# Kernel optimization log

Hardware: AMD Instinct MI355X
Metric: run time of the kernel (lower is better)

Reference implementation:

```python
import jax, jax.numpy as jnp
import numpy as np

B, T, D_IN, HID, D_OUT = 16, 4096, 256, 512, 256


def setup_inputs() -> dict:
    key = jax.random.key(0)
    k0, k1, k2, k3 = jax.random.split(key, 4)
    x = jax.random.normal(k0, (B, T, D_IN), dtype=jnp.float32)
    # nn.Linear default init ~ U(-1/sqrt(fan_in), 1/sqrt(fan_in)); approximate with scaled normal
    W_in = jax.random.normal(k1, (HID, D_IN), dtype=jnp.float32) / np.sqrt(D_IN)
    # hidden_ff.weight is explicitly set to diag(rand(hid_dim)) in the module
    W_h = jnp.diag(jax.random.uniform(k2, (HID,), dtype=jnp.float32))
    W_out = jax.random.normal(k3, (D_OUT, HID), dtype=jnp.float32) / np.sqrt(HID)
    return {"x": x, "W_in": W_in, "W_h": W_h, "W_out": W_out}


def reference(x, W_in, W_h, W_out):
    # x: [B, T, D_in]; W_in: [H, D_in]; W_h: [H, H]; W_out: [D_out, H]
    xp = jnp.einsum('btd,hd->bth', x, W_in)  # input projection, [B, T, H]

    def step(h, xt):
        # h_t = x_t + h_{t-1} @ W_h^T  (linear recurrence, h_0 = 0)
        h_next = xt + h @ W_h.T
        return h_next, h_next

    h0 = jnp.zeros((x.shape[0], W_h.shape[0]), dtype=x.dtype)
    _, hs = jax.lax.scan(step, h0, jnp.swapaxes(xp, 0, 1))  # hs: [T, B, H]
    hs = jnp.swapaxes(hs, 0, 1)  # [B, T, H]
    return jnp.einsum('bth,oh->bto', hs, W_out)  # [B, T, D_out]
```

## Files before the change

kernel.cpp:

```cpp
#include <hip/hip_runtime.h>
#include <hip/hip_bf16.h>
#include <stdint.h>

#define BATCH 16
#define SEQT  4096
#define DIN   256
#define HID   512
#define DOUT  256
#define M_TOT 65536
#define CLEN  128
#define NCHUNK 32

typedef short bf16x8 __attribute__((ext_vector_type(8)));
typedef float f32x4  __attribute__((ext_vector_type(4)));
typedef unsigned short u16;
typedef unsigned short u16x4 __attribute__((ext_vector_type(4)));
typedef unsigned int uint32;

__device__ __forceinline__ void ld_lds16(const void* g, void* l) {
    __builtin_amdgcn_global_load_lds(
        (const __attribute__((address_space(1))) void*)g,
        (__attribute__((address_space(3))) void*)l, 16, 0, 0);
}

__device__ __forceinline__ u16 f2bf_rne(float f) {
    uint32 v = __float_as_uint(f);
    v += 0x7FFFu + ((v >> 16) & 1u);
    return (u16)(v >> 16);
}

__device__ __forceinline__ float bf2f(u16 s) {
    return __uint_as_float((uint32)s << 16);
}

__device__ __forceinline__ void splitf(float f, u16& hi, u16& lo) {
    const uint32 u = __float_as_uint(f);
    hi = (u16)(u >> 16);
    lo = f2bf_rne(f - __uint_as_float(u & 0xFFFF0000u));
}

__global__ __launch_bounds__(256) void prep(
        const float* __restrict__ Wh, const float* __restrict__ Win,
        const float* __restrict__ Wout, float* __restrict__ wdiag,
        float* __restrict__ wpow, u16* __restrict__ Winhi,
        u16* __restrict__ Winlo, u16* __restrict__ Wouthi,
        u16* __restrict__ Woutlo) {
    const int bid = blockIdx.x, tid = threadIdx.x;
    if (bid == 0) {
        for (int h = tid; h < HID; h += 256) {
            const float wv = Wh[(size_t)h * HID + h];
            wdiag[h] = wv;
            float p = 1.f;
            for (int t = 0; t < CLEN; ++t) { p *= wv; wpow[t * HID + h] = p; }
        }
    } else if (bid <= 128) {
        const int f4 = (bid - 1) * 256 + tid;
        const f32x4 v = *(const f32x4*)(Win + (size_t)f4 * 4);
        u16x4 hv, lv;
#pragma unroll
        for (int k = 0; k < 4; ++k) { u16 a, b; splitf(v[k], a, b); hv[k] = a; lv[k] = b; }
        *(u16x4*)(Winhi + (size_t)f4 * 4) = hv;
        *(u16x4*)(Winlo + (size_t)f4 * 4) = lv;
    } else {
        const int f4 = (bid - 129) * 256 + tid;
        const f32x4 v = *(const f32x4*)(Wout + (size_t)f4 * 4);
        u16x4 hv, lv;
#pragma unroll
        for (int k = 0; k < 4; ++k) { u16 a, b; splitf(v[k], a, b); hv[k] = a; lv[k] = b; }
        *(u16x4*)(Wouthi + (size_t)f4 * 4) = hv;
        *(u16x4*)(Woutlo + (size_t)f4 * 4) = lv;
    }
}

__global__ __launch_bounds__(256, 2) void gemm1_scan(
        const float* __restrict__ X, const u16* __restrict__ Whi,
        const u16* __restrict__ Wlo, u16* __restrict__ localbf,
        float* __restrict__ L, const float* __restrict__ wdiag,
        const float* __restrict__ wpow) {
    __shared__ __align__(16) char smem[75776];
    u16*   Ah = (u16*)smem;
    u16*   Al = (u16*)(smem + 16384);
    u16*   Bh = (u16*)(smem + 32768);
    u16*   Bl = (u16*)(smem + 49152);
    float* st = (float*)smem;
    float* segT = (float*)(smem + 67584);
    float* segC = (float*)(smem + 71680);

    const int tid  = threadIdx.x;
    const int w    = tid >> 6;
    const int lane = tid & 63;

    const int bid  = blockIdx.x;
    const int xcd  = bid & 7;
    const int slot = bid >> 3;
    const int mBase = (xcd * 64 + (slot >> 2)) * 128;
    const int nBase = (slot & 3) * 128;

    const int wr = w >> 1, wc = w & 1;
    const int fr = lane & 15;
    const int kg = lane >> 4;

    const int bRow = lane >> 3;
    const int bCol = ((lane & 7) ^ bRow) * 8;

    f32x4 acc[4][4];
#pragma unroll
    for (int i = 0; i < 4; ++i)
#pragma unroll
        for (int j = 0; j < 4; ++j) acc[i][j] = (f32x4){0.f, 0.f, 0.f, 0.f};

    for (int k0 = 0; k0 < DIN; k0 += 64) {
#pragma unroll
        for (int i = 0; i < 4; ++i) {
            const int c = w * 4 + i;
            const int r = c * 8 + bRow;
            ld_lds16(Whi + (size_t)(nBase + r) * DIN + k0 + bCol, Bh + c * 512);
            ld_lds16(Wlo + (size_t)(nBase + r) * DIN + k0 + bCol, Bl + c * 512);
        }
#pragma unroll
        for (int it = 0; it < 4; ++it) {
            const int idx = it * 256 + tid;
            const int r  = idx >> 3;
            const int gl = idx & 7;
            const float* src = X + (size_t)(mBase + r) * DIN + k0 + gl * 8;
            const f32x4 v0 = *(const f32x4*)(src);
            const f32x4 v1 = *(const f32x4*)(src + 4);
            bf16x8 h8, l8;
#pragma unroll
            for (int e = 0; e < 4; ++e) {
                u16 a, b;
                splitf(v0[e], a, b); h8[e] = (short)a; l8[e] = (short)b;
                splitf(v1[e], a, b); h8[e + 4] = (short)a; l8[e + 4] = (short)b;
            }
            const int phys = r * 64 + ((gl ^ (r & 7)) * 8);
            *(bf16x8*)(Ah + phys) = h8;
            *(bf16x8*)(Al + phys) = l8;
        }
        __syncthreads();
#pragma unroll
        for (int ks = 0; ks < 2; ++ks) {
            const int colE = ks * 32 + kg * 8;
            bf16x8 ah[4], al[4], bh[4], bl[4];
#pragma unroll
            for (int f = 0; f < 4; ++f) {
                const int ra = wr * 64 + f * 16 + fr;
                const int pa = ra * 64 + (colE ^ ((fr & 7) << 3));
                ah[f] = *(const bf16x8*)(Ah + pa);
                al[f] = *(const bf16x8*)(Al + pa);
                const int rb = wc * 64 + f * 16 + fr;
                const int pb = rb * 64 + (colE ^ ((fr & 7) << 3));
                bh[f] = *(const bf16x8*)(Bh + pb);
                bl[f] = *(const bf16x8*)(Bl + pb);
            }
#pragma unroll
            for (int i = 0; i < 4; ++i)
#pragma unroll
                for (int j = 0; j < 4; ++j) {
                    acc[i][j] = __builtin_amdgcn_mfma_f32_16x16x32_bf16(ah[i], bh[j], acc[i][j], 0, 0, 0);
                    acc[i][j] = __builtin_amdgcn_mfma_f32_16x16x32_bf16(ah[i], bl[j], acc[i][j], 0, 0, 0);
                    acc[i][j] = __builtin_amdgcn_mfma_f32_16x16x32_bf16(al[i], bh[j], acc[i][j], 0, 0, 0);
                }
        }
        __syncthreads();
    }

#pragma unroll
    for (int i = 0; i < 4; ++i)
#pragma unroll
        for (int j = 0; j < 4; ++j)
#pragma unroll
            for (int rg = 0; rg < 4; ++rg)
                st[(wr * 64 + i * 16 + kg * 4 + rg) * 132 + wc * 64 + j * 16 + fr]
                    = acc[i][j][rg];
    __syncthreads();

    const int sseg = tid >> 5;
    const int cg   = (tid & 31) * 4;
    const f32x4 wv4 = *(const f32x4*)(wdiag + nBase + cg);

    f32x4 rr[16];
    {
        f32x4 run = (f32x4){0.f, 0.f, 0.f, 0.f};
#pragma unroll
        for (int i = 0; i < 16; ++i) {
            const f32x4 v = *(const f32x4*)&st[(sseg * 16 + i) * 132 + cg];
#pragma unroll
            for (int e = 0; e < 4; ++e) run[e] = fmaf(wv4[e], run[e], v[e]);
            rr[i] = run;
        }
        *(f32x4*)&segT[sseg * 128 + cg] = run;
    }
    __syncthreads();

    if (tid < 32) {
        const int c4 = tid * 4;
        const f32x4 w16 = *(const f32x4*)(wpow + 15 * HID + nBase + c4);
        f32x4 c = (f32x4){0.f, 0.f, 0.f, 0.f};
#pragma unroll
        for (int s2 = 0; s2 < 8; ++s2) {
            *(f32x4*)&segC[s2 * 128 + c4] = c;
            const f32x4 tv = *(const f32x4*)&segT[s2 * 128 + c4];
#pragma unroll
            for (int e = 0; e < 4; ++e) c[e] = fmaf(w16[e], c[e], tv[e]);
        }
        const int cI = (mBase >> 7) & (NCHUNK - 1);
        const int bI = mBase >> 12;
        *(f32x4*)&L[(cI * BATCH + bI) * HID + nBase + c4] = c;
    }
    __syncthreads();

    {
        const f32x4 cin = *(const f32x4*)&segC[sseg * 128 + cg];
        f32x4 p = wv4;
        u16* dst = localbf + (size_t)(mBase + sseg * 16) * HID + nBase + cg;
#pragma unroll
        for (int i = 0; i < 16; ++i) {
            u16x4 ob;
#pragma unroll
            for (int e = 0; e < 4; ++e)
                ob[e] = f2bf_rne(fmaf(p[e], cin[e], rr[i][e]));
            *(u16x4*)(dst + (size_t)i * HID) = ob;
#pragma unroll
            for (int e = 0; e < 4; ++e) p[e] *= wv4[e];
        }
    }
}

__global__ __launch_bounds__(256) void scan_carry(
        const float* __restrict__ L, const float* __restrict__ wpow,
        float* __restrict__ carry) {
    const int idx = blockIdx.x * 256 + threadIdx.x;
    const int h = idx & (HID - 1);
    const int b = idx >> 9;
    const float wf = wpow[(CLEN - 1) * HID + h];
    float H = 0.f;
    for (int c = 0; c < NCHUNK; ++c) {
        const int o = (c * BATCH + b) * HID + h;
        carry[o] = H;
        H = fmaf(wf, H, L[o]);
    }
}

__global__ __launch_bounds__(256, 2) void gemm2_fix(
        const u16* __restrict__ localbf, const u16* __restrict__ Bhi_g,
        const u16* __restrict__ Blo_g, const float* __restrict__ wpow,
        const float* __restrict__ carry, float* __restrict__ C) {
    __shared__ __align__(16) char smem[65536];
    u16* Ah = (u16*)smem;
    u16* Al = (u16*)(smem + 16384);
    u16* Bh = (u16*)(smem + 32768);
    u16* Bl = (u16*)(smem + 49152);

    const int tid  = threadIdx.x;
    const int w    = tid >> 6;
    const int lane = tid & 63;

    const int bid  = blockIdx.x;
    const int xcd  = bid & 7;
    const int slot = bid >> 3;
    const int mBase = (xcd * 64 + (slot >> 1)) * 128;
    const int nBase = (slot & 1) * 128;

    const int wr = w >> 1, wc = w & 1;
    const int fr = lane & 15;
    const int kg = lane >> 4;

    const int bRow = lane >> 3;
    const int bCol = ((lane & 7) ^ bRow) * 8;

    const int cI = (mBase >> 7) & (NCHUNK - 1);
    const int bI = mBase >> 12;
    const float* crow = carry + (size_t)(cI * BATCH + bI) * HID;

    f32x4 acc[4][4];
#pragma unroll
    for (int i = 0; i < 4; ++i)
#pragma unroll
        for (int j = 0; j < 4; ++j) acc[i][j] = (f32x4){0.f, 0.f, 0.f, 0.f};

    for (int k0 = 0; k0 < HID; k0 += 64) {
#pragma unroll
        for (int i = 0; i < 4; ++i) {
            const int c = w * 4 + i;
            const int r2 = c * 8 + bRow;
            ld_lds16(Bhi_g + (size_t)(nBase + r2) * HID + k0 + bCol, Bh + c * 512);
            ld_lds16(Blo_g + (size_t)(nBase + r2) * HID + k0 + bCol, Bl + c * 512);
        }
#pragma unroll
        for (int it = 0; it < 4; ++it) {
            const int idx = it * 256 + tid;
            const int r  = idx >> 3;
            const int gl = idx & 7;
            const int gm = mBase + r;
            const size_t col = (size_t)(k0 + gl * 8);
            const bf16x8 lv = *(const bf16x8*)(localbf + (size_t)gm * HID + col);
            const f32x4 p0 = *(const f32x4*)(wpow + (size_t)r * HID + col);
            const f32x4 p1 = *(const f32x4*)(wpow + (size_t)r * HID + col + 4);
            const f32x4 c0 = *(const f32x4*)(crow + col);
            const f32x4 c1 = *(const f32x4*)(crow + col + 4);
            bf16x8 h8, l8;
#pragma unroll
            for (int e = 0; e < 4; ++e) {
                const float f0 = fmaf(p0[e], c0[e], bf2f((u16)lv[e]));
                const float f1 = fmaf(p1[e], c1[e], bf2f((u16)lv[e + 4]));
                u16 a, b;
                splitf(f0, a, b); h8[e] = (short)a; l8[e] = (short)b;
                splitf(f1, a, b); h8[e + 4] = (short)a; l8[e + 4] = (short)b;
            }
            const int phys = r * 64 + ((gl ^ (r & 7)) * 8);
            *(bf16x8*)(Ah + phys) = h8;
            *(bf16x8*)(Al + phys) = l8;
        }
        __syncthreads();
#pragma unroll
        for (int ks = 0; ks < 2; ++ks) {
            const int colE = ks * 32 + kg * 8;
            bf16x8 ah[4], al[4], bh[4], bl[4];
#pragma unroll
            for (int f = 0; f < 4; ++f) {
                const int ra = wr * 64 + f * 16 + fr;
                const int pa = ra * 64 + (colE ^ ((fr & 7) << 3));
                ah[f] = *(const bf16x8*)(Ah + pa);
                al[f] = *(const bf16x8*)(Al + pa);
                const int rb = wc * 64 + f * 16 + fr;
                const int pb = rb * 64 + (colE ^ ((fr & 7) << 3));
                bh[f] = *(const bf16x8*)(Bh + pb);
                bl[f] = *(const bf16x8*)(Bl + pb);
            }
#pragma unroll
            for (int i = 0; i < 4; ++i)
#pragma unroll
                for (int j = 0; j < 4; ++j) {
                    acc[i][j] = __builtin_amdgcn_mfma_f32_16x16x32_bf16(ah[i], bh[j], acc[i][j], 0, 0, 0);
                    acc[i][j] = __builtin_amdgcn_mfma_f32_16x16x32_bf16(ah[i], bl[j], acc[i][j], 0, 0, 0);
                    acc[i][j] = __builtin_amdgcn_mfma_f32_16x16x32_bf16(al[i], bh[j], acc[i][j], 0, 0, 0);
                }
        }
        __syncthreads();
    }

#pragma unroll
    for (int i = 0; i < 4; ++i) {
        const size_t row0 = (size_t)mBase + wr * 64 + i * 16 + kg * 4;
#pragma unroll
        for (int j = 0; j < 4; ++j) {
            const int col = nBase + wc * 64 + j * 16 + fr;
#pragma unroll
            for (int rg = 0; rg < 4; ++rg)
                C[(row0 + rg) * DOUT + col] = acc[i][j][rg];
        }
    }
}

extern "C" void kernel_launch(void* const* d_in, const int* in_sizes, int n_in,
                              void* d_out, int out_size, void* d_ws, size_t ws_size,
                              hipStream_t stream) {
    const float* x     = (const float*)d_in[0];
    const float* W_in  = (const float*)d_in[1];
    const float* W_h   = (const float*)d_in[2];
    const float* W_out = (const float*)d_in[3];
    float* out = (float*)d_out;

    char* ws = (char*)d_ws;
    u16*   localbf = (u16*)(ws);
    float* L       = (float*)(ws + 134217728);
    float* carry   = (float*)(ws + 135266304);
    float* wpow    = (float*)(ws + 136314880);
    float* wdiag   = (float*)(ws + 136577024);
    u16*   Winhi   = (u16*)(ws + 136579072);
    u16*   Winlo   = (u16*)(ws + 136841216);
    u16*   Wouthi  = (u16*)(ws + 137103360);
    u16*   Woutlo  = (u16*)(ws + 137365504);

    prep<<<257, 256, 0, stream>>>(W_h, W_in, W_out, wdiag, wpow,
                                  Winhi, Winlo, Wouthi, Woutlo);
    gemm1_scan<<<2048, 256, 0, stream>>>(x, Winhi, Winlo, localbf, L, wdiag, wpow);
    scan_carry<<<32, 256, 0, stream>>>(L, wpow, carry);
    gemm2_fix<<<1024, 256, 0, stream>>>(localbf, Wouthi, Woutlo, wpow, carry, out);
}
```

Before: 128.0 us.

## Register-prefetch next K tile in gemm1 and compute segment carries redundantly per thread

Replaces the direct global-to-LDS loads of the weight tiles and the synchronous X load/split with a register prefetch. The next K slice is loaded into registers while MFMA runs on the current slice, which is meant to overlap global latency with compute. It also removes the single-warp carry pass and its extra barrier: every thread recomputes the 8-segment carry chain from segT and picks its own incoming carry, which drops the segC buffer and shrinks LDS. The cost is higher register pressure from the prefetch buffers under launch_bounds(256,2), plus some redundant carry arithmetic.

```diff
diff --git a/kernel.cpp b/kernel.cpp
--- a/kernel.cpp
+++ b/kernel.cpp
@@ -77,14 +77,13 @@
         const u16* __restrict__ Wlo, u16* __restrict__ localbf,
         float* __restrict__ L, const float* __restrict__ wdiag,
         const float* __restrict__ wpow) {
-    __shared__ __align__(16) char smem[75776];
+    __shared__ __align__(16) char smem[71680];
     u16*   Ah = (u16*)smem;
     u16*   Al = (u16*)(smem + 16384);
     u16*   Bh = (u16*)(smem + 32768);
     u16*   Bl = (u16*)(smem + 49152);
     float* st = (float*)smem;
     float* segT = (float*)(smem + 67584);
-    float* segC = (float*)(smem + 71680);
 
     const int tid  = threadIdx.x;
     const int w    = tid >> 6;
@@ -109,34 +108,56 @@
 #pragma unroll
         for (int j = 0; j < 4; ++j) acc[i][j] = (f32x4){0.f, 0.f, 0.f, 0.f};
 
-    for (int k0 = 0; k0 < DIN; k0 += 64) {
+    f32x4 ap0[4], ap1[4];
+    bf16x8 bhp[4], blp[4];
+
+    auto LOADK = [&](int k0) {
 #pragma unroll
         for (int i = 0; i < 4; ++i) {
             const int c = w * 4 + i;
             const int r = c * 8 + bRow;
-            ld_lds16(Whi + (size_t)(nBase + r) * DIN + k0 + bCol, Bh + c * 512);
-            ld_lds16(Wlo + (size_t)(nBase + r) * DIN + k0 + bCol, Bl + c * 512);
+            bhp[i] = *(const bf16x8*)(Whi + (size_t)(nBase + r) * DIN + k0 + bCol);
+            blp[i] = *(const bf16x8*)(Wlo + (size_t)(nBase + r) * DIN + k0 + bCol);
         }
 #pragma unroll
         for (int it = 0; it < 4; ++it) {
             const int idx = it * 256 + tid;
-            const int r  = idx >> 3;
-            const int gl = idx & 7;
+            const int r = idx >> 3, gl = idx & 7;
             const float* src = X + (size_t)(mBase + r) * DIN + k0 + gl * 8;
-            const f32x4 v0 = *(const f32x4*)(src);
-            const f32x4 v1 = *(const f32x4*)(src + 4);
+            ap0[it] = *(const f32x4*)(src);
+            ap1[it] = *(const f32x4*)(src + 4);
+        }
+    };
+    auto WRITEK = [&]() {
+#pragma unroll
+        for (int i = 0; i < 4; ++i) {
+            const int c = w * 4 + i;
+            *(bf16x8*)(Bh + c * 512 + lane * 8) = bhp[i];
+            *(bf16x8*)(Bl + c * 512 + lane * 8) = blp[i];
+        }
+#pragma unroll
+        for (int it = 0; it < 4; ++it) {
+            const int idx = it * 256 + tid;
+            const int r = idx >> 3, gl = idx & 7;
             bf16x8 h8, l8;
 #pragma unroll
             for (int e = 0; e < 4; ++e) {
                 u16 a, b;
-                splitf(v0[e], a, b); h8[e] = (short)a; l8[e] = (short)b;
-                splitf(v1[e], a, b); h8[e + 4] = (short)a; l8[e + 4] = (short)b;
+                splitf(ap0[it][e], a, b); h8[e] = (short)a; l8[e] = (short)b;
+                splitf(ap1[it][e], a, b); h8[e + 4] = (short)a; l8[e + 4] = (short)b;
             }
             const int phys = r * 64 + ((gl ^ (r & 7)) * 8);
             *(bf16x8*)(Ah + phys) = h8;
             *(bf16x8*)(Al + phys) = l8;
         }
+    };
+
+    LOADK(0);
+#pragma unroll
+    for (int kk = 0; kk < 4; ++kk) {
+        WRITEK();
         __syncthreads();
+        if (kk < 3) LOADK((kk + 1) * 64);
 #pragma unroll
         for (int ks = 0; ks < 2; ++ks) {
             const int colE = ks * 32 + kg * 8;
@@ -192,25 +213,22 @@
     }
     __syncthreads();
 
-    if (tid < 32) {
-        const int c4 = tid * 4;
-        const f32x4 w16 = *(const f32x4*)(wpow + 15 * HID + nBase + c4);
+    {
+        const f32x4 w16 = *(const f32x4*)(wpow + 15 * HID + nBase + cg);
         f32x4 c = (f32x4){0.f, 0.f, 0.f, 0.f};
-#pragma unroll
-        for (int s2 = 0; s2 < 8; ++s2) {
-            *(f32x4*)&segC[s2 * 128 + c4] = c;
-            const f32x4 tv = *(const f32x4*)&segT[s2 * 128 + c4];
+        f32x4 cin = (f32x4){0.f, 0.f, 0.f, 0.f};
+#pragma unroll
+        for (int s = 0; s < 8; ++s) {
+            if (s == sseg) cin = c;
+            const f32x4 tv = *(const f32x4*)&segT[s * 128 + cg];
 #pragma unroll
             for (int e = 0; e < 4; ++e) c[e] = fmaf(w16[e], c[e], tv[e]);
         }
-        const int cI = (mBase >> 7) & (NCHUNK - 1);
-        const int bI = mBase >> 12;
-        *(f32x4*)&L[(cI * BATCH + bI) * HID + nBase + c4] = c;
-    }
-    __syncthreads();
-
-    {
-        const f32x4 cin = *(const f32x4*)&segC[sseg * 128 + cg];
+        if (sseg == 7) {
+            const int cI = (mBase >> 7) & (NCHUNK - 1);
+            const int bI = mBase >> 12;
+            *(f32x4*)&L[(cI * BATCH + bI) * HID + nBase + cg] = c;
+        }
         f32x4 p = wv4;
         u16* dst = localbf + (size_t)(mBase + sseg * 16) * HID + nBase + cg;
 #pragma unroll
```

Measured after the change: 129.5 us. Within noise of the previous version (+1.2%).

## Do chunk scan in registers with shuffles, shrink LDS for higher occupancy

Applied to the files above, without the earlier changes.

The K-step drops from 64 to 32, which halves the A/B LDS tiles, and the fp32 staging tile is replaced by a bf16 one. Total shared memory falls from about 74KB to about 35KB and the launch bound rises to 4 blocks per CU. The intra-chunk diagonal recurrence now runs directly on MFMA accumulator registers, using lane shuffles and precomputed powers of w, with a single cross-warp carry passed through LDS. The bf16 output is written through a staging buffer so global stores are coalesced. In exchange there are more loop iterations and barriers, extra register pressure from the power arrays, and numerical differences in how the powers are computed.

```diff
diff --git a/kernel.cpp b/kernel.cpp
--- a/kernel.cpp
+++ b/kernel.cpp
@@ -38,6 +38,8 @@
     hi = (u16)(u >> 16);
     lo = f2bf_rne(f - __uint_as_float(u & 0xFFFF0000u));
 }
+
+__device__ __forceinline__ int sfun(int r) { return (r ^ (r >> 2)) & 3; }
 
 __global__ __launch_bounds__(256) void prep(
         const float* __restrict__ Wh, const float* __restrict__ Win,
@@ -72,19 +74,17 @@
     }
 }
 
-__global__ __launch_bounds__(256, 2) void gemm1_scan(
+__global__ __launch_bounds__(256, 4) void gemm1_scan(
         const float* __restrict__ X, const u16* __restrict__ Whi,
         const u16* __restrict__ Wlo, u16* __restrict__ localbf,
-        float* __restrict__ L, const float* __restrict__ wdiag,
-        const float* __restrict__ wpow) {
-    __shared__ __align__(16) char smem[75776];
-    u16*   Ah = (u16*)smem;
-    u16*   Al = (u16*)(smem + 16384);
-    u16*   Bh = (u16*)(smem + 32768);
-    u16*   Bl = (u16*)(smem + 49152);
-    float* st = (float*)smem;
-    float* segT = (float*)(smem + 67584);
-    float* segC = (float*)(smem + 71680);
+        float* __restrict__ L, const float* __restrict__ wdiag) {
+    __shared__ __align__(16) char smem[35328];
+    u16*   Ah  = (u16*)smem;
+    u16*   Al  = (u16*)(smem + 8192);
+    u16*   Bh  = (u16*)(smem + 16384);
+    u16*   Bl  = (u16*)(smem + 24576);
+    u16*   stb = (u16*)smem;
+    float* xw  = (float*)(smem + 34816);
 
     const int tid  = threadIdx.x;
     const int w    = tid >> 6;
@@ -100,8 +100,13 @@
     const int fr = lane & 15;
     const int kg = lane >> 4;
 
-    const int bRow = lane >> 3;
-    const int bCol = ((lane & 7) ^ bRow) * 8;
+    const int r_a = tid >> 1;
+    const int h_a = tid & 1;
+    const int s_a = sfun(r_a);
+
+    const int rl  = lane >> 2;
+    const int pg  = lane & 3;
+    const int lgb = pg ^ sfun(rl);
 
     f32x4 acc[4][4];
 #pragma unroll
@@ -109,119 +114,147 @@
 #pragma unroll
         for (int j = 0; j < 4; ++j) acc[i][j] = (f32x4){0.f, 0.f, 0.f, 0.f};
 
-    for (int k0 = 0; k0 < DIN; k0 += 64) {
-#pragma unroll
-        for (int i = 0; i < 4; ++i) {
-            const int c = w * 4 + i;
-            const int r = c * 8 + bRow;
-            ld_lds16(Whi + (size_t)(nBase + r) * DIN + k0 + bCol, Bh + c * 512);
-            ld_lds16(Wlo + (size_t)(nBase + r) * DIN + k0 + bCol, Bl + c * 512);
-        }
-#pragma unroll
-        for (int it = 0; it < 4; ++it) {
-            const int idx = it * 256 + tid;
-            const int r  = idx >> 3;
-            const int gl = idx & 7;
-            const float* src = X + (size_t)(mBase + r) * DIN + k0 + gl * 8;
+    for (int kk = 0; kk < 8; ++kk) {
+        const int k0 = kk * 32;
+#pragma unroll
+        for (int i = 0; i < 2; ++i) {
+            const int c = w * 2 + i;
+            const int row = nBase + c * 16 + rl;
+            ld_lds16(Whi + (size_t)row * DIN + k0 + lgb * 8, Bh + c * 512);
+            ld_lds16(Wlo + (size_t)row * DIN + k0 + lgb * 8, Bl + c * 512);
+        }
+        {
+            const float* src = X + (size_t)(mBase + r_a) * DIN + k0 + h_a * 16;
             const f32x4 v0 = *(const f32x4*)(src);
             const f32x4 v1 = *(const f32x4*)(src + 4);
-            bf16x8 h8, l8;
+            const f32x4 v2 = *(const f32x4*)(src + 8);
+            const f32x4 v3 = *(const f32x4*)(src + 12);
+            bf16x8 h0, l0, h1, l1;
 #pragma unroll
             for (int e = 0; e < 4; ++e) {
                 u16 a, b;
-                splitf(v0[e], a, b); h8[e] = (short)a; l8[e] = (short)b;
-                splitf(v1[e], a, b); h8[e + 4] = (short)a; l8[e + 4] = (short)b;
-            }
-            const int phys = r * 64 + ((gl ^ (r & 7)) * 8);
-            *(bf16x8*)(Ah + phys) = h8;
-            *(bf16x8*)(Al + phys) = l8;
+                splitf(v0[e], a, b); h0[e] = (short)a; l0[e] = (short)b;
+                splitf(v1[e], a, b); h0[e + 4] = (short)a; l0[e + 4] = (short)b;
+                splitf(v2[e], a, b); h1[e] = (short)a; l1[e] = (short)b;
+                splitf(v3[e], a, b); h1[e + 4] = (short)a; l1[e + 4] = (short)b;
+            }
+            u16* arow = Ah + r_a * 32;
+            u16* arol = Al + r_a * 32;
+            const int g0 = (2 * h_a) ^ s_a, g1 = (2 * h_a + 1) ^ s_a;
+            *(bf16x8*)(arow + g0 * 8) = h0;
+            *(bf16x8*)(arow + g1 * 8) = h1;
+            *(bf16x8*)(arol + g0 * 8) = l0;
+            *(bf16x8*)(arol + g1 * 8) = l1;
         }
         __syncthreads();
-#pragma unroll
-        for (int ks = 0; ks < 2; ++ks) {
-            const int colE = ks * 32 + kg * 8;
-            bf16x8 ah[4], al[4], bh[4], bl[4];
-#pragma unroll
-            for (int f = 0; f < 4; ++f) {
-                const int ra = wr * 64 + f * 16 + fr;
-                const int pa = ra * 64 + (colE ^ ((fr & 7) << 3));
-                ah[f] = *(const bf16x8*)(Ah + pa);
-                al[f] = *(const bf16x8*)(Al + pa);
-                const int rb = wc * 64 + f * 16 + fr;
-                const int pb = rb * 64 + (colE ^ ((fr & 7) << 3));
-                bh[f] = *(const bf16x8*)(Bh + pb);
-                bl[f] = *(const bf16x8*)(Bl + pb);
-            }
-#pragma unroll
-            for (int i = 0; i < 4; ++i)
-#pragma unroll
-                for (int j = 0; j < 4; ++j) {
-                    acc[i][j] = __builtin_amdgcn_mfma_f32_16x16x32_bf16(ah[i], bh[j], acc[i][j], 0, 0, 0);
-                    acc[i][j] = __builtin_amdgcn_mfma_f32_16x16x32_bf16(ah[i], bl[j], acc[i][j], 0, 0, 0);
-                    acc[i][j] = __builtin_amdgcn_mfma_f32_16x16x32_bf16(al[i], bh[j], acc[i][j], 0, 0, 0);
-                }
-        }
+
+        const int sfr = sfun(fr);
+        bf16x8 ah[4], al[4], bh[4], bl[4];
+#pragma unroll
+        for (int f = 0; f < 4; ++f) {
+            const int sa = (wr * 64 + f * 16 + fr) * 32 + ((kg ^ sfr) * 8);
+            ah[f] = *(const bf16x8*)(Ah + sa);
+            al[f] = *(const bf16x8*)(Al + sa);
+            const int sb = (wc * 64 + f * 16 + fr) * 32 + ((kg ^ sfr) * 8);
+            bh[f] = *(const bf16x8*)(Bh + sb);
+            bl[f] = *(const bf16x8*)(Bl + sb);
+        }
+#pragma unroll
+        for (int i = 0; i < 4; ++i)
+#pragma unroll
+            for (int j = 0; j < 4; ++j) {
+                acc[i][j] = __builtin_amdgcn_mfma_f32_16x16x32_bf16(ah[i], bh[j], acc[i][j], 0, 0, 0);
+                acc[i][j] = __builtin_amdgcn_mfma_f32_16x16x32_bf16(ah[i], bl[j], acc[i][j], 0, 0, 0);
+                acc[i][j] = __builtin_amdgcn_mfma_f32_16x16x32_bf16(al[i], bh[j], acc[i][j], 0, 0, 0);
+            }
         __syncthreads();
     }
 
-#pragma unroll
-    for (int i = 0; i < 4; ++i)
-#pragma unroll
-        for (int j = 0; j < 4; ++j)
-#pragma unroll
-            for (int rg = 0; rg < 4; ++rg)
-                st[(wr * 64 + i * 16 + kg * 4 + rg) * 132 + wc * 64 + j * 16 + fr]
-                    = acc[i][j][rg];
+    float w1[4], w2[4], w3[4], w4[4], w8[4], w16[4];
+#pragma unroll
+    for (int j = 0; j < 4; ++j) {
+        const float wv = wdiag[nBase + wc * 64 + j * 16 + fr];
+        w1[j] = wv; w2[j] = wv * wv; w3[j] = w2[j] * wv; w4[j] = w2[j] * w2[j];
+        w8[j] = w4[j] * w4[j]; w16[j] = w8[j] * w8[j];
+    }
+    float Bst[4] = {0.f, 0.f, 0.f, 0.f};
+#pragma unroll
+    for (int i = 0; i < 4; ++i) {
+#pragma unroll
+        for (int j = 0; j < 4; ++j) {
+            const float l0 = acc[i][j][0];
+            const float l1 = fmaf(w1[j], l0, acc[i][j][1]);
+            const float l2 = fmaf(w1[j], l1, acc[i][j][2]);
+            const float l3 = fmaf(w1[j], l2, acc[i][j][3]);
+            const float x0 = __shfl(l3, fr);
+            const float x1 = __shfl(l3, fr + 16);
+            const float x2 = __shfl(l3, fr + 32);
+            const float x3 = __shfl(l3, fr + 48);
+            float s = Bst[j];
+            float S = s;
+            s = fmaf(w4[j], s, x0); S = (kg == 1) ? s : S;
+            s = fmaf(w4[j], s, x1); S = (kg == 2) ? s : S;
+            s = fmaf(w4[j], s, x2); S = (kg == 3) ? s : S;
+            s = fmaf(w4[j], s, x3);
+            Bst[j] = s;
+            acc[i][j][0] = fmaf(w1[j], S, l0);
+            acc[i][j][1] = fmaf(w2[j], S, l1);
+            acc[i][j][2] = fmaf(w3[j], S, l2);
+            acc[i][j][3] = fmaf(w4[j], S, l3);
+        }
+    }
+    if (wr == 0 && kg == 0) {
+#pragma unroll
+        for (int j = 0; j < 4; ++j) xw[wc * 64 + j * 16 + fr] = Bst[j];
+    }
     __syncthreads();
-
-    const int sseg = tid >> 5;
-    const int cg   = (tid & 31) * 4;
-    const f32x4 wv4 = *(const f32x4*)(wdiag + nBase + cg);
-
-    f32x4 rr[16];
-    {
-        f32x4 run = (f32x4){0.f, 0.f, 0.f, 0.f};
-#pragma unroll
-        for (int i = 0; i < 16; ++i) {
-            const f32x4 v = *(const f32x4*)&st[(sseg * 16 + i) * 132 + cg];
-#pragma unroll
-            for (int e = 0; e < 4; ++e) run[e] = fmaf(wv4[e], run[e], v[e]);
-            rr[i] = run;
-        }
-        *(f32x4*)&segT[sseg * 128 + cg] = run;
-    }
-    __syncthreads();
-
-    if (tid < 32) {
-        const int c4 = tid * 4;
-        const f32x4 w16 = *(const f32x4*)(wpow + 15 * HID + nBase + c4);
-        f32x4 c = (f32x4){0.f, 0.f, 0.f, 0.f};
-#pragma unroll
-        for (int s2 = 0; s2 < 8; ++s2) {
-            *(f32x4*)&segC[s2 * 128 + c4] = c;
-            const f32x4 tv = *(const f32x4*)&segT[s2 * 128 + c4];
-#pragma unroll
-            for (int e = 0; e < 4; ++e) c[e] = fmaf(w16[e], c[e], tv[e]);
-        }
+    if (wr == 1) {
         const int cI = (mBase >> 7) & (NCHUNK - 1);
         const int bI = mBase >> 12;
-        *(f32x4*)&L[(cI * BATCH + bI) * HID + nBase + c4] = c;
+#pragma unroll
+        for (int j = 0; j < 4; ++j) {
+            const float cin = xw[wc * 64 + j * 16 + fr];
+            float wkg = 1.f;
+            if (kg & 1) wkg *= w4[j];
+            if (kg & 2) wkg *= w8[j];
+            float f = wkg;
+#pragma unroll
+            for (int i = 0; i < 4; ++i) {
+                const float g = f * cin;
+                acc[i][j][0] = fmaf(w1[j], g, acc[i][j][0]);
+                acc[i][j][1] = fmaf(w2[j], g, acc[i][j][1]);
+                acc[i][j][2] = fmaf(w3[j], g, acc[i][j][2]);
+                acc[i][j][3] = fmaf(w4[j], g, acc[i][j][3]);
+                f *= w16[j];
+            }
+            if (kg == 0) {
+                const float w32 = w16[j] * w16[j];
+                const float w64 = w32 * w32;
+                L[(cI * BATCH + bI) * HID + nBase + wc * 64 + j * 16 + fr]
+                    = fmaf(w64, cin, Bst[j]);
+            }
+        }
     }
     __syncthreads();
 
+#pragma unroll
+    for (int i = 0; i < 4; ++i)
+#pragma unroll
+        for (int j = 0; j < 4; ++j)
+#pragma unroll
+            for (int rg = 0; rg < 4; ++rg)
+                stb[(wr * 64 + i * 16 + kg * 4 + rg) * 136
+                    + wc * 64 + j * 16 + fr] = f2bf_rne(acc[i][j][rg]);
+    __syncthreads();
+
     {
-        const f32x4 cin = *(const f32x4*)&segC[sseg * 128 + cg];
-        f32x4 p = wv4;
-        u16* dst = localbf + (size_t)(mBase + sseg * 16) * HID + nBase + cg;
-#pragma unroll
-        for (int i = 0; i < 16; ++i) {
-            u16x4 ob;
-#pragma unroll
-            for (int e = 0; e < 4; ++e)
-                ob[e] = f2bf_rne(fmaf(p[e], cin[e], rr[i][e]));
-            *(u16x4*)(dst + (size_t)i * HID) = ob;
-#pragma unroll
-            for (int e = 0; e < 4; ++e) p[e] *= wv4[e];
+        const int rr2 = tid >> 4;
+        const int cl  = (tid & 15) * 8;
+#pragma unroll
+        for (int p = 0; p < 8; ++p) {
+            const int row = p * 16 + rr2;
+            const bf16x8 v = *(const bf16x8*)(stb + row * 136 + cl);
+            *(bf16x8*)(localbf + (size_t)(mBase + row) * HID + nBase + cl) = v;
         }
     }
 }
@@ -374,7 +407,7 @@
 
     prep<<<257, 256, 0, stream>>>(W_h, W_in, W_out, wdiag, wpow,
                                   Winhi, Winlo, Wouthi, Woutlo);
-    gemm1_scan<<<2048, 256, 0, stream>>>(x, Winhi, Winlo, localbf, L, wdiag, wpow);
+    gemm1_scan<<<2048, 256, 0, stream>>>(x, Winhi, Winlo, localbf, L, wdiag);
     scan_carry<<<32, 256, 0, stream>>>(L, wpow, carry);
     gemm2_fix<<<1024, 256, 0, stream>>>(localbf, Wouthi, Woutlo, wpow, carry, out);
 }
```

Measured after the change: 156.6 us. +22.4%, slower.

## Double gemm1_scan block to 512 threads with 16-step scan segments

Applied to the files above, without the earlier changes.

Raises gemm1_scan from 256 to 512 threads per block. Each wave now covers a 64x32 output tile instead of 64x64, and the chunk scan is split into 16 segments of 8 rows instead of 8 segments of 16. The serial carry pass that only 32 threads ran is replaced by every thread redundantly scanning the 16 segment totals, which removes one barrier and the segC buffer. The aim is more waves per CU and a shorter serial scan, at the cost of less register reuse per wave in the MFMA loop and redundant carry arithmetic.

```diff
diff --git a/kernel.cpp b/kernel.cpp
--- a/kernel.cpp
+++ b/kernel.cpp
@@ -72,7 +72,7 @@
     }
 }
 
-__global__ __launch_bounds__(256, 2) void gemm1_scan(
+__global__ __launch_bounds__(512, 2) void gemm1_scan(
         const float* __restrict__ X, const u16* __restrict__ Whi,
         const u16* __restrict__ Wlo, u16* __restrict__ localbf,
         float* __restrict__ L, const float* __restrict__ wdiag,
@@ -84,7 +84,6 @@
     u16*   Bl = (u16*)(smem + 49152);
     float* st = (float*)smem;
     float* segT = (float*)(smem + 67584);
-    float* segC = (float*)(smem + 71680);
 
     const int tid  = threadIdx.x;
     const int w    = tid >> 6;
@@ -96,30 +95,31 @@
     const int mBase = (xcd * 64 + (slot >> 2)) * 128;
     const int nBase = (slot & 3) * 128;
 
-    const int wr = w >> 1, wc = w & 1;
+    const int wr = w >> 2;
+    const int wc = w & 3;
     const int fr = lane & 15;
     const int kg = lane >> 4;
 
     const int bRow = lane >> 3;
     const int bCol = ((lane & 7) ^ bRow) * 8;
 
-    f32x4 acc[4][4];
+    f32x4 acc[4][2];
 #pragma unroll
     for (int i = 0; i < 4; ++i)
 #pragma unroll
-        for (int j = 0; j < 4; ++j) acc[i][j] = (f32x4){0.f, 0.f, 0.f, 0.f};
+        for (int j = 0; j < 2; ++j) acc[i][j] = (f32x4){0.f, 0.f, 0.f, 0.f};
 
     for (int k0 = 0; k0 < DIN; k0 += 64) {
 #pragma unroll
-        for (int i = 0; i < 4; ++i) {
-            const int c = w * 4 + i;
+        for (int i = 0; i < 2; ++i) {
+            const int c = w * 2 + i;
             const int r = c * 8 + bRow;
             ld_lds16(Whi + (size_t)(nBase + r) * DIN + k0 + bCol, Bh + c * 512);
             ld_lds16(Wlo + (size_t)(nBase + r) * DIN + k0 + bCol, Bl + c * 512);
         }
 #pragma unroll
-        for (int it = 0; it < 4; ++it) {
-            const int idx = it * 256 + tid;
+        for (int it = 0; it < 2; ++it) {
+            const int idx = it * 512 + tid;
             const int r  = idx >> 3;
             const int gl = idx & 7;
             const float* src = X + (size_t)(mBase + r) * DIN + k0 + gl * 8;
@@ -140,22 +140,25 @@
 #pragma unroll
         for (int ks = 0; ks < 2; ++ks) {
             const int colE = ks * 32 + kg * 8;
-            bf16x8 ah[4], al[4], bh[4], bl[4];
+            bf16x8 ah[4], al[4], bh[2], bl[2];
 #pragma unroll
             for (int f = 0; f < 4; ++f) {
                 const int ra = wr * 64 + f * 16 + fr;
                 const int pa = ra * 64 + (colE ^ ((fr & 7) << 3));
                 ah[f] = *(const bf16x8*)(Ah + pa);
                 al[f] = *(const bf16x8*)(Al + pa);
-                const int rb = wc * 64 + f * 16 + fr;
+            }
+#pragma unroll
+            for (int j = 0; j < 2; ++j) {
+                const int rb = wc * 32 + j * 16 + fr;
                 const int pb = rb * 64 + (colE ^ ((fr & 7) << 3));
-                bh[f] = *(const bf16x8*)(Bh + pb);
-                bl[f] = *(const bf16x8*)(Bl + pb);
+                bh[j] = *(const bf16x8*)(Bh + pb);
+                bl[j] = *(const bf16x8*)(Bl + pb);
             }
 #pragma unroll
             for (int i = 0; i < 4; ++i)
 #pragma unroll
-                for (int j = 0; j < 4; ++j) {
+                for (int j = 0; j < 2; ++j) {
                     acc[i][j] = __builtin_amdgcn_mfma_f32_16x16x32_bf16(ah[i], bh[j], acc[i][j], 0, 0, 0);
                     acc[i][j] = __builtin_amdgcn_mfma_f32_16x16x32_bf16(ah[i], bl[j], acc[i][j], 0, 0, 0);
                     acc[i][j] = __builtin_amdgcn_mfma_f32_16x16x32_bf16(al[i], bh[j], acc[i][j], 0, 0, 0);
@@ -167,10 +170,10 @@
 #pragma unroll
     for (int i = 0; i < 4; ++i)
 #pragma unroll
-        for (int j = 0; j < 4; ++j)
+        for (int j = 0; j < 2; ++j)
 #pragma unroll
             for (int rg = 0; rg < 4; ++rg)
-                st[(wr * 64 + i * 16 + kg * 4 + rg) * 132 + wc * 64 + j * 16 + fr]
+                st[(wr * 64 + i * 16 + kg * 4 + rg) * 132 + wc * 32 + j * 16 + fr]
                     = acc[i][j][rg];
     __syncthreads();
 
@@ -178,12 +181,12 @@
     const int cg   = (tid & 31) * 4;
     const f32x4 wv4 = *(const f32x4*)(wdiag + nBase + cg);
 
-    f32x4 rr[16];
+    f32x4 rr[8];
     {
         f32x4 run = (f32x4){0.f, 0.f, 0.f, 0.f};
 #pragma unroll
-        for (int i = 0; i < 16; ++i) {
-            const f32x4 v = *(const f32x4*)&st[(sseg * 16 + i) * 132 + cg];
+        for (int i = 0; i < 8; ++i) {
+            const f32x4 v = *(const f32x4*)&st[(sseg * 8 + i) * 132 + cg];
 #pragma unroll
             for (int e = 0; e < 4; ++e) run[e] = fmaf(wv4[e], run[e], v[e]);
             rr[i] = run;
@@ -192,29 +195,26 @@
     }
     __syncthreads();
 
-    if (tid < 32) {
-        const int c4 = tid * 4;
-        const f32x4 w16 = *(const f32x4*)(wpow + 15 * HID + nBase + c4);
+    {
+        const f32x4 w8 = *(const f32x4*)(wpow + 7 * HID + nBase + cg);
         f32x4 c = (f32x4){0.f, 0.f, 0.f, 0.f};
-#pragma unroll
-        for (int s2 = 0; s2 < 8; ++s2) {
-            *(f32x4*)&segC[s2 * 128 + c4] = c;
-            const f32x4 tv = *(const f32x4*)&segT[s2 * 128 + c4];
-#pragma unroll
-            for (int e = 0; e < 4; ++e) c[e] = fmaf(w16[e], c[e], tv[e]);
-        }
-        const int cI = (mBase >> 7) & (NCHUNK - 1);
-        const int bI = mBase >> 12;
-        *(f32x4*)&L[(cI * BATCH + bI) * HID + nBase + c4] = c;
-    }
-    __syncthreads();
-
-    {
-        const f32x4 cin = *(const f32x4*)&segC[sseg * 128 + cg];
+        f32x4 cin = (f32x4){0.f, 0.f, 0.f, 0.f};
+#pragma unroll
+        for (int s = 0; s < 16; ++s) {
+            if (s == sseg) cin = c;
+            const f32x4 tv = *(const f32x4*)&segT[s * 128 + cg];
+#pragma unroll
+            for (int e = 0; e < 4; ++e) c[e] = fmaf(w8[e], c[e], tv[e]);
+        }
+        if (sseg == 15) {
+            const int cI = (mBase >> 7) & (NCHUNK - 1);
+            const int bI = mBase >> 12;
+            *(f32x4*)&L[(cI * BATCH + bI) * HID + nBase + cg] = c;
+        }
         f32x4 p = wv4;
-        u16* dst = localbf + (size_t)(mBase + sseg * 16) * HID + nBase + cg;
-#pragma unroll
-        for (int i = 0; i < 16; ++i) {
+        u16* dst = localbf + (size_t)(mBase + sseg * 8) * HID + nBase + cg;
+#pragma unroll
+        for (int i = 0; i < 8; ++i) {
             u16x4 ob;
 #pragma unroll
             for (int e = 0; e < 4; ++e)
@@ -374,7 +374,7 @@
 
     prep<<<257, 256, 0, stream>>>(W_h, W_in, W_out, wdiag, wpow,
                                   Winhi, Winlo, Wouthi, Woutlo);
-    gemm1_scan<<<2048, 256, 0, stream>>>(x, Winhi, Winlo, localbf, L, wdiag, wpow);
+    gemm1_scan<<<2048, 512, 0, stream>>>(x, Winhi, Winlo, localbf, L, wdiag, wpow);
     scan_carry<<<32, 256, 0, stream>>>(L, wpow, carry);
     gemm2_fix<<<1024, 256, 0, stream>>>(localbf, Wouthi, Woutlo, wpow, carry, out);
 }
```

Result: slower. 132.3 us (+3.4%).
